# Optimization experiments

Hardware: AMD Instinct MI355X
Metric: run time of the kernel (lower is better)

Reference implementation:

```python
import jax, jax.numpy as jnp
import numpy as np

NUM_SLOTS = 168   # hour-of-week time slots
NUM_CATS = 2048   # category vocabulary
BATCH, SEQ = 512, 200


def setup_inputs() -> dict:
    key = jax.random.key(0)
    k1, k2 = jax.random.split(key)
    inputs_hour = jax.random.randint(k1, (BATCH, SEQ), 0, NUM_SLOTS)
    catid_time_matrix = jax.random.normal(k2, (NUM_SLOTS, NUM_CATS), dtype=jnp.float32)
    return {"inputs_hour": inputs_hour, "catid_time_matrix": catid_time_matrix}


def reference(inputs_hour, catid_time_matrix):
    # softmax over categories (dim=1), then gather rows for each hour index.
    probs = jax.nn.softmax(catid_time_matrix, axis=1)          # [slots, cats]
    return probs[inputs_hour]                                   # [batch, seq, cats]
```

## Files before the change

kernel.cpp:

```cpp
#include <hip/hip_runtime.h>
#include <hip/hip_bf16.h>

#define NUM_SLOTS 168
#define NUM_CATS 2048
#define BATCH 512
#define SEQ 200
#define ROWS_PER_BLOCK 50

typedef float v4f __attribute__((ext_vector_type(4)));

__global__ void softmax_rows_kernel(const float* __restrict__ mat,
                                    float* __restrict__ probs) {
    const int row = blockIdx.x;
    const float* r = mat + row * NUM_CATS;
    float* o = probs + row * NUM_CATS;
    const int t = threadIdx.x;

    float vals[8];
    float mx = -INFINITY;
#pragma unroll
    for (int j = 0; j < 8; ++j) {
        vals[j] = r[t + j * 256];
        mx = fmaxf(mx, vals[j]);
    }
#pragma unroll
    for (int off = 32; off >= 1; off >>= 1) mx = fmaxf(mx, __shfl_xor(mx, off));

    __shared__ float redmax[4];
    __shared__ float redsum[4];
    const int wave = t >> 6;
    if ((t & 63) == 0) redmax[wave] = mx;
    __syncthreads();
    mx = fmaxf(fmaxf(redmax[0], redmax[1]), fmaxf(redmax[2], redmax[3]));

    float sum = 0.0f;
#pragma unroll
    for (int j = 0; j < 8; ++j) {
        vals[j] = expf(vals[j] - mx);
        sum += vals[j];
    }
#pragma unroll
    for (int off = 32; off >= 1; off >>= 1) sum += __shfl_xor(sum, off);
    if ((t & 63) == 0) redsum[wave] = sum;
    __syncthreads();
    sum = redsum[0] + redsum[1] + redsum[2] + redsum[3];

    const float inv = 1.0f / sum;
#pragma unroll
    for (int j = 0; j < 8; ++j) o[t + j * 256] = vals[j] * inv;
}

__global__ void __launch_bounds__(256)
gather_rows_kernel(const int* __restrict__ hours,
                   const v4f* __restrict__ probs,
                   v4f* __restrict__ out) {
    const int t = threadIdx.x;
    const int row0 = blockIdx.x * ROWS_PER_BLOCK;
#pragma unroll 2
    for (int r = 0; r < ROWS_PER_BLOCK; ++r) {
        const int row = row0 + r;
        const int h = hours[row];
        const v4f* __restrict__ src = probs + (h << 9);
        v4f* __restrict__ dst = out + ((size_t)row << 9);
        const v4f a = src[t];
        const v4f b = src[t + 256];
        __builtin_nontemporal_store(a, &dst[t]);
        __builtin_nontemporal_store(b, &dst[t + 256]);
    }
}

extern "C" void kernel_launch(void* const* d_in, const int* in_sizes, int n_in,
                              void* d_out, int out_size, void* d_ws, size_t ws_size,
                              hipStream_t stream) {
    const int* inputs_hour = (const int*)d_in[0];
    const float* catid_time_matrix = (const float*)d_in[1];
    float* out = (float*)d_out;
    float* probs = (float*)d_ws;

    softmax_rows_kernel<<<NUM_SLOTS, 256, 0, stream>>>(catid_time_matrix, probs);

    gather_rows_kernel<<<(BATCH * SEQ) / ROWS_PER_BLOCK, 256, 0, stream>>>(
        inputs_hour, (const v4f*)probs, (v4f*)out);
}
```

Measured before the change: 175.2 us.

## Bucket output rows by hour index to reuse gathered probability rows

Adds a counting sort of the hour indices: a histogram, a prefix sum and an atomic scatter, so rows sharing the same hour become contiguous. The gather kernel then reloads the probability row only when the hour changes within a chunk and otherwise reuses the registers. This cuts redundant reads of the small probs table. The cost is three extra kernel launches, global atomics, and a nondeterministic output row order that scatters the stores. The workload is dominated by the ~420MB of output writes, so the saved reads (mostly L2 hits already) may not offset the added launches.

```diff
diff --git a/kernel.cpp b/kernel.cpp
--- a/kernel.cpp
+++ b/kernel.cpp
@@ -5,16 +5,25 @@
 #define NUM_CATS 2048
 #define BATCH 512
 #define SEQ 200
-#define ROWS_PER_BLOCK 50
+#define NROWS (BATCH * SEQ)
+#define CHUNK 100
 
 typedef float v4f __attribute__((ext_vector_type(4)));
 
+#define WS_PROBS 0
+#define WS_COUNTS 344064
+#define WS_CURSORS 344408
+#define WS_SORTED 344576
+
 __global__ void softmax_rows_kernel(const float* __restrict__ mat,
-                                    float* __restrict__ probs) {
+                                    float* __restrict__ probs,
+                                    int* __restrict__ counts) {
     const int row = blockIdx.x;
+    const int t = threadIdx.x;
+    if (row == 0 && t < NUM_SLOTS) counts[t] = 0;
+
     const float* r = mat + row * NUM_CATS;
     float* o = probs + row * NUM_CATS;
-    const int t = threadIdx.x;
 
     float vals[8];
     float mx = -INFINITY;
@@ -50,20 +59,64 @@
     for (int j = 0; j < 8; ++j) o[t + j * 256] = vals[j] * inv;
 }
 
+__global__ void __launch_bounds__(256) count_kernel(const int* __restrict__ hours,
+                                                    int* __restrict__ counts) {
+    __shared__ int hist[NUM_SLOTS];
+    const int t = threadIdx.x;
+    if (t < NUM_SLOTS) hist[t] = 0;
+    __syncthreads();
+    const int base = blockIdx.x * 1024 + t;
+#pragma unroll
+    for (int k = 0; k < 4; ++k) atomicAdd(&hist[hours[base + k * 256]], 1);
+    __syncthreads();
+    if (t < NUM_SLOTS) atomicAdd(&counts[t], hist[t]);
+}
+
+__global__ void __launch_bounds__(256) prefix_kernel(const int* __restrict__ counts,
+                                                     int* __restrict__ cursors) {
+    __shared__ int c[NUM_SLOTS];
+    const int t = threadIdx.x;
+    if (t < NUM_SLOTS) c[t] = counts[t];
+    __syncthreads();
+    if (t == 0) {
+        int s = 0;
+        for (int i = 0; i < NUM_SLOTS; ++i) { const int v = c[i]; c[i] = s; s += v; }
+    }
+    __syncthreads();
+    if (t < NUM_SLOTS) cursors[t] = c[t];
+}
+
+__global__ void __launch_bounds__(256) scatter_kernel(const int* __restrict__ hours,
+                                                      int* __restrict__ cursors,
+                                                      int* __restrict__ sorted) {
+    const int i = blockIdx.x * 256 + threadIdx.x;
+    const int h = hours[i];
+    const int pos = atomicAdd(&cursors[h], 1);
+    sorted[pos] = (h << 17) | i;
+}
+
 __global__ void __launch_bounds__(256)
-gather_rows_kernel(const int* __restrict__ hours,
-                   const v4f* __restrict__ probs,
-                   v4f* __restrict__ out) {
+gather_bucketed_kernel(const int* __restrict__ sorted,
+                       const v4f* __restrict__ probs,
+                       v4f* __restrict__ out) {
+    __shared__ int lst[CHUNK];
     const int t = threadIdx.x;
-    const int row0 = blockIdx.x * ROWS_PER_BLOCK;
-#pragma unroll 2
-    for (int r = 0; r < ROWS_PER_BLOCK; ++r) {
-        const int row = row0 + r;
-        const int h = hours[row];
-        const v4f* __restrict__ src = probs + (h << 9);
+    const int base = blockIdx.x * CHUNK;
+    if (t < CHUNK) lst[t] = sorted[base + t];
+    __syncthreads();
+
+    int cur_h = -1;
+    v4f a, b;
+    for (int i = 0; i < CHUNK; ++i) {
+        const int v = lst[i];
+        const int h = v >> 17;
+        const int row = v & 0x1FFFF;
+        if (h != cur_h) {
+            a = probs[(h << 9) + t];
+            b = probs[(h << 9) + t + 256];
+            cur_h = h;
+        }
         v4f* __restrict__ dst = out + ((size_t)row << 9);
-        const v4f a = src[t];
-        const v4f b = src[t + 256];
         __builtin_nontemporal_store(a, &dst[t]);
         __builtin_nontemporal_store(b, &dst[t + 256]);
     }
@@ -75,10 +128,16 @@
     const int* inputs_hour = (const int*)d_in[0];
     const float* catid_time_matrix = (const float*)d_in[1];
     float* out = (float*)d_out;
-    float* probs = (float*)d_ws;
 
-    softmax_rows_kernel<<<NUM_SLOTS, 256, 0, stream>>>(catid_time_matrix, probs);
+    float* probs = (float*)d_ws + WS_PROBS;
+    int* counts = (int*)d_ws + WS_COUNTS;
+    int* cursors = (int*)d_ws + WS_CURSORS;
+    int* sorted = (int*)d_ws + WS_SORTED;
 
-    gather_rows_kernel<<<(BATCH * SEQ) / ROWS_PER_BLOCK, 256, 0, stream>>>(
-        inputs_hour, (const v4f*)probs, (v4f*)out);
+    softmax_rows_kernel<<<NUM_SLOTS, 256, 0, stream>>>(catid_time_matrix, probs, counts);
+    count_kernel<<<NROWS / 1024, 256, 0, stream>>>(inputs_hour, counts);
+    prefix_kernel<<<1, 256, 0, stream>>>(counts, cursors);
+    scatter_kernel<<<NROWS / 256, 256, 0, stream>>>(inputs_hour, cursors, sorted);
+    gather_bucketed_kernel<<<NROWS / CHUNK, 256, 0, stream>>>(
+        sorted, (const v4f*)probs, (v4f*)out);
 }
```

After: 246.9 us. 1.41x slower.
